# Performance work log

Hardware: AMD Instinct MI355X
Metric: run time of the kernel (lower is better)

## Reference

```python
import jax, jax.numpy as jnp
import numpy as np

IMG = 224          # image_size
FMAP = (56, 56)    # feature_map_dims (AdaptiveAvgPool2d((56,56)))
K_REWEIGHT = 3     # self.n_reweight
BLUR_RADIUS = 4    # KNNGaussianBlur(4): kernel 9, sigma 4


def _cdist(a, b):
    # Euclidean pairwise distance, [Na, D] x [Nb, D] -> [Na, Nb]
    a2 = jnp.sum(a * a, axis=1, keepdims=True)            # [Na,1]
    b2 = jnp.sum(b * b, axis=1, keepdims=True).T          # [1,Nb]
    d2 = a2 + b2 - 2.0 * (a @ b.T)
    return jnp.sqrt(jnp.maximum(d2, 0.0))


def _gaussian_blur(x):
    # x: [1,1,H,W]; torchvision GaussianBlur(kernel=9, sigma=4), reflect pad
    r, sigma = BLUR_RADIUS, float(BLUR_RADIUS)
    t = jnp.arange(2 * r + 1, dtype=x.dtype) - r
    g = jnp.exp(-(t * t) / (2.0 * sigma * sigma))
    g = g / jnp.sum(g)
    k2d = jnp.outer(g, g)[None, None]                     # [1,1,9,9]
    xp = jnp.pad(x, ((0, 0), (0, 0), (r, r), (r, r)), mode='reflect')
    return jax.lax.conv_general_dilated(
        xp, k2d, window_strides=(1, 1), padding='VALID',
        dimension_numbers=('NCHW', 'OIHW', 'NCHW'))


def setup_inputs() -> dict:
    key = jax.random.key(0)
    k1, k2 = jax.random.split(key)
    patch = jax.random.normal(k1, (FMAP[0] * FMAP[1], 768), dtype=jnp.float32)
    patch_lib = jax.random.normal(k2, (16384, 768), dtype=jnp.float32)
    mean = jnp.zeros((), dtype=jnp.float32)
    std = jnp.ones((), dtype=jnp.float32)
    return {"patch": patch, "patch_lib": patch_lib, "mean": mean, "std": std}


def reference(patch, patch_lib, mean, std):
    # normalization (method_name != 'Point_MAE' branch)
    p = (patch - mean) / std                               # [N, D]

    dist = _cdist(p, patch_lib)                            # [N, Nlib]
    min_val = jnp.min(dist, axis=1)                        # [N]
    min_idx = jnp.argmin(dist, axis=1)                     # [N]
    s_idx = jnp.argmax(min_val)
    s_star = jnp.max(min_val)

    m_test = p[s_idx]                                      # [D]
    m_star = patch_lib[min_idx[s_idx]]                     # [D]

    # distances of m_star to whole bank, k smallest
    w_dist = jnp.sqrt(jnp.maximum(
        jnp.sum((patch_lib - m_star) ** 2, axis=1), 0.0))  # [Nlib]
    _, nn_idx = jax.lax.top_k(-w_dist, K_REWEIGHT)         # smallest k
    m_star_knn = jnp.linalg.norm(
        m_test[None, :] - patch_lib[nn_idx[1:]], axis=1)   # [k-1]

    D_sqrt = jnp.sqrt(jnp.asarray(patch.shape[1], dtype=p.dtype))
    w = 1.0 - jnp.exp(s_star / D_sqrt) / jnp.sum(jnp.exp(m_star_knn / D_sqrt))
    s = w * s_star

    s_map = min_val.reshape(1, 1, *FMAP)
    s_map = jax.image.resize(s_map, (1, 1, IMG, IMG), method='bilinear')
    s_map = _gaussian_blur(s_map)
    return s, s_map
```

## Files before the change

kernel.cpp:

```cpp
#include <hip/hip_runtime.h>
#include <hip/hip_bf16.h>
#include <stdint.h>

#define N_PATCH 3136
#define N_PATCH_PAD 3328
#define N_LIB   16384
#define DIM     768
#define IMGSZ   224
#define FM      56

#define TILE 256
#define BK 32
#define KT 24
#define MT 13
#define NTILES 64

#define TAILB 64
#define D2_MARGIN 8.0f

typedef __bf16 bf16_t;
typedef __bf16 bf16x8 __attribute__((ext_vector_type(8)));
typedef __bf16 bf16x4_v __attribute__((ext_vector_type(4)));
typedef float  f32x4  __attribute__((ext_vector_type(4)));

#define FLT_MAX_ 3.402823466e+38f

struct Scal {
  unsigned long long approx_max_pack;
  unsigned long long cand_pack[64];
  int cand[64];
  int cand_count;
  int bar[4];
};

__device__ __forceinline__ float wave_reduce_sum(float v) {
#pragma unroll
  for (int s = 32; s > 0; s >>= 1) v += __shfl_xor(v, s, 64);
  return v;
}

__device__ __forceinline__ float wave_reduce_min(float v) {
#pragma unroll
  for (int s = 32; s > 0; s >>= 1) v = fminf(v, __shfl_xor(v, s, 64));
  return v;
}

__device__ __forceinline__ unsigned long long shfl_xor_u64(unsigned long long v, int mask) {
  unsigned lo = (unsigned)v, hi = (unsigned)(v >> 32);
  lo = __shfl_xor(lo, mask, 64);
  hi = __shfl_xor(hi, mask, 64);
  return ((unsigned long long)hi << 32) | lo;
}

__device__ __forceinline__ void async16(const bf16_t* g, bf16_t* l) {
  __builtin_amdgcn_global_load_lds(
      (const __attribute__((address_space(1))) unsigned int*)g,
      (__attribute__((address_space(3))) unsigned int*)l, 16, 0, 0);
}

__device__ __forceinline__ void grid_bar(int* ctr, int nb) {
  __syncthreads();
  if (threadIdx.x == 0) {
    __threadfence();
    atomicAdd(ctr, 1);
    while (atomicAdd(ctr, 0) < nb) __builtin_amdgcn_s_sleep(8);
    __threadfence();
  }
  __syncthreads();
}

__device__ __forceinline__ float bf16u_to_f(unsigned short u) {
  return __uint_as_float(((unsigned)u) << 16);
}

__global__ void prep_kernel(const float* __restrict__ patch, const float* __restrict__ lib,
                            const float* __restrict__ meanp, const float* __restrict__ stdp,
                            bf16_t* __restrict__ pb, bf16_t* __restrict__ lb,
                            float* __restrict__ a2, float* __restrict__ b2, Scal* sc) {
  int t = threadIdx.x;
  int lane = t & 63;
  if (blockIdx.x == 0) {
    if (t < 64) sc->cand_pack[t] = ~0ULL;
    if (t == 64) { sc->approx_max_pack = 0ULL; sc->cand_count = 0; }
    if (t >= 65 && t < 69) sc->bar[t - 65] = 0;
  }
  if (blockIdx.x < N_PATCH / 4) {
    int row = blockIdx.x * 4 + (t >> 6);
    float mu = meanp[0], sd = stdp[0];
    float acc = 0.f;
#pragma unroll
    for (int k = 0; k < 3; k++) {
      float4 v = ((const float4*)(patch + (size_t)row * DIM))[lane + 64 * k];
      v.x = (v.x - mu) / sd; v.y = (v.y - mu) / sd;
      v.z = (v.z - mu) / sd; v.w = (v.w - mu) / sd;
      bf16x4_v o = {(__bf16)v.x, (__bf16)v.y, (__bf16)v.z, (__bf16)v.w};
      *(bf16x4_v*)(pb + (size_t)row * DIM + (lane + 64 * k) * 4) = o;
      acc += v.x*v.x + v.y*v.y + v.z*v.z + v.w*v.w;
    }
    acc = wave_reduce_sum(acc);
    if (lane == 0) a2[row] = acc;
  } else {
    int row = (blockIdx.x - N_PATCH / 4) * 4 + (t >> 6);
    float acc = 0.f;
#pragma unroll
    for (int k = 0; k < 3; k++) {
      float4 v = ((const float4*)(lib + (size_t)row * DIM))[lane + 64 * k];
      bf16x4_v o = {(__bf16)v.x, (__bf16)v.y, (__bf16)v.z, (__bf16)v.w};
      *(bf16x4_v*)(lb + (size_t)row * DIM + (lane + 64 * k) * 4) = o;
      acc += v.x*v.x + v.y*v.y + v.z*v.z + v.w*v.w;
    }
    acc = wave_reduce_sum(acc);
    if (lane == 0) b2[row] = acc;
  }
}

__global__ __launch_bounds__(512, 2)
void gemm_min_kernel(const bf16_t* __restrict__ pb, const bf16_t* __restrict__ lb,
                     const float* __restrict__ a2, const float* __restrict__ b2,
                     float* __restrict__ part) {
  __shared__ __align__(16) bf16_t As[4][TILE * BK];
  __shared__ __align__(16) bf16_t Bs[4][TILE * BK];

  const int t = threadIdx.x;
  const int wave = t >> 6;
  const int lane = t & 63;
  const int l15 = lane & 15;
  const int quad = lane >> 4;
  const int wm = (wave >> 2) * 128;
  const int wn = (wave & 3) * 64;

  const int lid = blockIdx.x;
  const int xcd = lid & 7;
  const int slot = lid >> 3;
  const int ntile = xcd + 8 * (slot / MT);
  const int mtile = slot % MT;
  const int m0 = mtile * TILE;
  const int n0 = ntile * TILE;

  int ra0 = m0 + (t >> 2);        if (ra0 > N_PATCH - 1) ra0 = N_PATCH - 1;
  int ra1 = m0 + 128 + (t >> 2);  if (ra1 > N_PATCH - 1) ra1 = N_PATCH - 1;
  const bf16_t* gA0 = pb + (size_t)ra0 * DIM + (t & 3) * 8;
  const bf16_t* gA1 = pb + (size_t)ra1 * DIM + (t & 3) * 8;
  const bf16_t* gB0 = lb + (size_t)(n0 + (t >> 2)) * DIM + (t & 3) * 8;
  const bf16_t* gB1 = gB0 + (size_t)128 * DIM;

  auto stage = [&](int kt, int s) {
    const size_t ko = (size_t)kt * BK;
    async16(gA0 + ko, &As[s][0] + (size_t)t * 8);
    async16(gA1 + ko, &As[s][0] + 4096 + (size_t)t * 8);
    async16(gB0 + ko, &Bs[s][0] + (size_t)t * 8);
    async16(gB1 + ko, &Bs[s][0] + 4096 + (size_t)t * 8);
  };

  f32x4 acc[8][4];
#pragma unroll
  for (int mi = 0; mi < 8; mi++)
#pragma unroll
    for (int ni = 0; ni < 4; ni++) { f32x4 z = {0.f,0.f,0.f,0.f}; acc[mi][ni] = z; }

  stage(0, 0); stage(1, 1); stage(2, 2);

  auto compute = [&](int s) {
    const bf16_t* Ab = &As[s][0];
    const bf16_t* Bb = &Bs[s][0];
    bf16x8 afr[8], bfr[4];
#pragma unroll
    for (int ni = 0; ni < 4; ni++)
      bfr[ni] = *(const bf16x8*)(Bb + (wn + ni * 16 + l15) * BK + quad * 8);
#pragma unroll
    for (int mi = 0; mi < 8; mi++)
      afr[mi] = *(const bf16x8*)(Ab + (wm + mi * 16 + l15) * BK + quad * 8);
    __builtin_amdgcn_s_setprio(1);
#pragma unroll
    for (int mi = 0; mi < 8; mi++)
#pragma unroll
      for (int ni = 0; ni < 4; ni++)
        acc[mi][ni] = __builtin_amdgcn_mfma_f32_16x16x32_bf16(afr[mi], bfr[ni],
                                                              acc[mi][ni], 0, 0, 0);
    __builtin_amdgcn_s_setprio(0);
  };

  for (int k = 0; k < KT - 3; ++k) {
    asm volatile("s_waitcnt vmcnt(8)" ::: "memory");
    __builtin_amdgcn_s_barrier();
    asm volatile("" ::: "memory");
    stage(k + 3, (k + 3) & 3);
    compute(k & 3);
  }
  asm volatile("s_waitcnt vmcnt(8)" ::: "memory");
  __builtin_amdgcn_s_barrier();
  asm volatile("" ::: "memory");
  compute((KT - 3) & 3);

  asm volatile("s_waitcnt vmcnt(4)" ::: "memory");
  __builtin_amdgcn_s_barrier();
  asm volatile("" ::: "memory");
  compute((KT - 2) & 3);

  asm volatile("s_waitcnt vmcnt(0)" ::: "memory");
  __builtin_amdgcn_s_barrier();
  asm volatile("" ::: "memory");
  compute((KT - 1) & 3);

  __syncthreads();
  unsigned* smin = (unsigned*)&As[0][0];
  if (t < 256) smin[t] = 0xffffffffu;
  __syncthreads();

  float b2n[4];
#pragma unroll
  for (int ni = 0; ni < 4; ni++) b2n[ni] = b2[n0 + wn + ni * 16 + l15];

#pragma unroll
  for (int mi = 0; mi < 8; mi++) {
#pragma unroll
    for (int r = 0; r < 4; r++) {
      int rloc = wm + mi * 16 + quad * 4 + r;
      int mrow = m0 + rloc;
      float a2v = a2[mrow < N_PATCH ? mrow : (N_PATCH - 1)];
      float best = a2v + b2n[0] - 2.0f * acc[mi][0][r];
#pragma unroll
      for (int ni = 1; ni < 4; ni++)
        best = fminf(best, a2v + b2n[ni] - 2.0f * acc[mi][ni][r]);
      best = fmaxf(best, 0.0f);
#pragma unroll
      for (int s = 1; s < 16; s <<= 1)
        best = fminf(best, __shfl_xor(best, s, 64));
      if (l15 == 0) atomicMin(&smin[rloc], __float_as_uint(best));
    }
  }
  __syncthreads();
  if (t < 256) part[(size_t)ntile * N_PATCH_PAD + m0 + t] = __uint_as_float(smin[t]);
}

__device__ __forceinline__ void wave_pick(const Scal* sc, int cnt, int lane,
                                          int* srow, float* sstar, int* ms) {
  unsigned long long pk = 0ULL;
  int rowv = 0, msv = 0;
  if (lane < cnt) {
    unsigned long long cp = sc->cand_pack[lane];
    rowv = sc->cand[lane];
    msv = (int)(cp & 0xffffffffu);
    pk = (cp & 0xffffffff00000000ULL) | (unsigned)(0xffffffffu - (unsigned)rowv);
  }
  unsigned long long m = pk;
#pragma unroll
  for (int s = 1; s < 64; s <<= 1) {
    unsigned long long o = shfl_xor_u64(m, s);
    if (o > m) m = o;
  }
  unsigned long long mask = __ballot(pk == m && lane < cnt);
  int wl = (int)(__ffsll((long long)mask) - 1);
  *srow = __shfl(rowv, wl, 64);
  *ms   = __shfl(msv, wl, 64);
  *sstar = sqrtf(__uint_as_float((unsigned)(m >> 32)));
}

__global__ __launch_bounds__(256, 2)
void tail_kernel(const float* __restrict__ part, float* __restrict__ min_val,
                 const float* __restrict__ patch, const float* __restrict__ lib,
                 const bf16_t* __restrict__ lb,
                 const float* __restrict__ meanp, const float* __restrict__ stdp,
                 Scal* __restrict__ sc, float* __restrict__ wdist2,
                 float* __restrict__ out0, float* __restrict__ outmap) {
  __shared__ union {
    unsigned long long sl[768];
    float rs[40 * 40];
  } sm;
  __shared__ float redbuf[4];
  __shared__ int s_cnt;

  const int t = threadIdx.x;
  const int b = blockIdx.x;
  const int wave = t >> 6, lane = t & 63;

  {
    int row = b * 256 + t;
    if (row < N_PATCH) {
      float m = FLT_MAX_;
#pragma unroll 8
      for (int nt = 0; nt < NTILES; nt++)
        m = fminf(m, part[(size_t)nt * N_PATCH_PAD + row]);
      float v = sqrtf(m);
      min_val[row] = v;
      unsigned long long mp = (((unsigned long long)__float_as_uint(v)) << 32) |
                              (unsigned)(0xffffffffu - (unsigned)row);
      atomicMax(&sc->approx_max_pack, mp);
    }
  }
  grid_bar(&sc->bar[0], TAILB);

  if (b == 0) {
    float amax = __uint_as_float((unsigned)(atomicMax(&sc->approx_max_pack, 0ULL) >> 32));
    for (int i = t; i < N_PATCH; i += 256) {
      if (min_val[i] >= amax - 0.05f) {
        int p = atomicAdd(&sc->cand_count, 1);
        if (p < 64) sc->cand[p] = i;
      }
    }
  }
  grid_bar(&sc->bar[1], TAILB);

  if (t == 0) s_cnt = atomicAdd(&sc->cand_count, 0);
  __syncthreads();
  int cnt = s_cnt; if (cnt > 64) cnt = 64;

  {
    float mu = meanp[0], sd = stdp[0];
    for (int c = 0; c < cnt; c++) {
      int row = sc->cand[c];
      float pv_ = (t < NTILES) ? part[(size_t)t * N_PATCH_PAD + row] : FLT_MAX_;
      pv_ = wave_reduce_min(pv_);
      if (lane == 0) redbuf[wave] = pv_;
      __syncthreads();
      float bmin = fminf(fminf(redbuf[0], redbuf[1]), fminf(redbuf[2], redbuf[3]));
      __syncthreads();

      float4 pv[3];
#pragma unroll
      for (int k = 0; k < 3; k++) {
        float4 v = ((const float4*)(patch + (size_t)row * DIM))[lane + 64 * k];
        v.x = (v.x - mu) / sd; v.y = (v.y - mu) / sd;
        v.z = (v.z - mu) / sd; v.w = (v.w - mu) / sd;
        pv[k] = v;
      }
      int nt = b;
      float pmin = part[(size_t)nt * N_PATCH_PAD + row];
      if (pmin <= bmin + D2_MARGIN) {
        unsigned long long best = ~0ULL;
        int jb = nt * 256 + wave * 64;
        for (int rr = 0; rr < 64; rr++) {
          int j = jb + rr;
          const float4* pl = (const float4*)(lib + (size_t)j * DIM);
          float acc = 0.f;
#pragma unroll
          for (int k = 0; k < 3; k++) {
            float4 l = pl[lane + 64 * k];
            float dx = pv[k].x - l.x, dy = pv[k].y - l.y;
            float dz = pv[k].z - l.z, dw = pv[k].w - l.w;
            acc += dx*dx + dy*dy + dz*dz + dw*dw;
          }
          acc = wave_reduce_sum(acc);
          unsigned long long pk = (((unsigned long long)__float_as_uint(acc)) << 32) | (unsigned)j;
          if (pk < best) best = pk;
        }
        if (lane == 0) atomicMin(&sc->cand_pack[c], best);
      }
    }
  }
  grid_bar(&sc->bar[2], TAILB);

  {
    int srow_, ms; float ss_;
    wave_pick(sc, cnt, lane, &srow_, &ss_, &ms);
    float pm[12];
    const ushort4* pms = (const ushort4*)(lb + (size_t)ms * DIM);
#pragma unroll
    for (int k = 0; k < 3; k++) {
      ushort4 u = pms[lane + 64 * k];
      pm[k*4+0] = bf16u_to_f(u.x); pm[k*4+1] = bf16u_to_f(u.y);
      pm[k*4+2] = bf16u_to_f(u.z); pm[k*4+3] = bf16u_to_f(u.w);
    }
    int jbase = b * 256 + wave * 64;
    for (int rr = 0; rr < 64; rr += 2) {
      int j0 = jbase + rr, j1 = j0 + 1;
      const ushort4* r0 = (const ushort4*)(lb + (size_t)j0 * DIM);
      const ushort4* r1 = (const ushort4*)(lb + (size_t)j1 * DIM);
      float a0 = 0.f, a1 = 0.f;
#pragma unroll
      for (int k = 0; k < 3; k++) {
        ushort4 u0 = r0[lane + 64 * k];
        ushort4 u1 = r1[lane + 64 * k];
        float d;
        d = bf16u_to_f(u0.x) - pm[k*4+0]; a0 += d * d;
        d = bf16u_to_f(u0.y) - pm[k*4+1]; a0 += d * d;
        d = bf16u_to_f(u0.z) - pm[k*4+2]; a0 += d * d;
        d = bf16u_to_f(u0.w) - pm[k*4+3]; a0 += d * d;
        d = bf16u_to_f(u1.x) - pm[k*4+0]; a1 += d * d;
        d = bf16u_to_f(u1.y) - pm[k*4+1]; a1 += d * d;
        d = bf16u_to_f(u1.z) - pm[k*4+2]; a1 += d * d;
        d = bf16u_to_f(u1.w) - pm[k*4+3]; a1 += d * d;
      }
      a0 = wave_reduce_sum(a0);
      a1 = wave_reduce_sum(a1);
      if (lane == 0) { wdist2[j0] = a0; wdist2[j1] = a1; }
    }
  }
  grid_bar(&sc->bar[3], TAILB);

  if (b == 0) {
    unsigned long long b0 = ~0ULL, b1 = ~0ULL, b2 = ~0ULL;
    for (int j = t; j < N_LIB; j += 256) {
      unsigned long long pk = (((unsigned long long)__float_as_uint(wdist2[j])) << 32) | (unsigned)j;
      if (pk < b0)      { b2 = b1; b1 = b0; b0 = pk; }
      else if (pk < b1) { b2 = b1; b1 = pk; }
      else if (pk < b2) { b2 = pk; }
    }
    sm.sl[t * 3 + 0] = b0; sm.sl[t * 3 + 1] = b1; sm.sl[t * 3 + 2] = b2;
    __syncthreads();
    if (t >= 64) return;

    unsigned long long c0 = ~0ULL, c1 = ~0ULL, c2 = ~0ULL;
#pragma unroll
    for (int e = 0; e < 12; e++) {
      unsigned long long pk = sm.sl[t * 12 + e];
      if (pk < c0)      { c2 = c1; c1 = c0; c0 = pk; }
      else if (pk < c1) { c2 = c1; c1 = pk; }
      else if (pk < c2) { c2 = pk; }
    }
    unsigned long long res1 = 0, res2 = 0;
#pragma unroll
    for (int r = 0; r < 3; r++) {
      unsigned long long m = c0;
#pragma unroll
      for (int s = 1; s < 64; s <<= 1) {
        unsigned long long o = shfl_xor_u64(m, s);
        if (o < m) m = o;
      }
      if (r == 1) res1 = m;
      if (r == 2) res2 = m;
      if (c0 == m) { c0 = c1; c1 = c2; c2 = ~0ULL; }
    }
    int nA = (int)(res1 & 0xffffffffu);
    int nB = (int)(res2 & 0xffffffffu);

    int srow, ms2; float sstar;
    wave_pick(sc, cnt, t, &srow, &sstar, &ms2);

    float mu = meanp[0], sd = stdp[0];
    float accA = 0.f, accB = 0.f;
#pragma unroll
    for (int k = 0; k < 3; k++) {
      float4 p4 = ((const float4*)(patch + (size_t)srow * DIM))[t + 64 * k];
      float4 a4 = ((const float4*)(lib + (size_t)nA * DIM))[t + 64 * k];
      float4 b4 = ((const float4*)(lib + (size_t)nB * DIM))[t + 64 * k];
      float px = (p4.x - mu) / sd, py = (p4.y - mu) / sd;
      float pz = (p4.z - mu) / sd, pw = (p4.w - mu) / sd;
      float dax = px - a4.x, day = py - a4.y, daz = pz - a4.z, daw = pw - a4.w;
      float dbx = px - b4.x, dby = py - b4.y, dbz = pz - b4.z, dbw = pw - b4.w;
      accA += dax*dax + day*day + daz*daz + daw*daw;
      accB += dbx*dbx + dby*dby + dbz*dbz + dbw*dbw;
    }
    accA = wave_reduce_sum(accA);
    accB = wave_reduce_sum(accB);
    if (t == 0) {
      float dsq = sqrtf((float)DIM);
      float d1 = sqrtf(accA), d2v = sqrtf(accB);
      float w = 1.0f - expf(sstar / dsq) / (expf(d1 / dsq) + expf(d2v / dsq));
      out0[0] = w * sstar;
    }
    return;
  }

  if (b > 49) return;
  {
    int tile = b - 1;
    int bx = tile % 7, by = tile / 7;
    int ox0 = bx * 32, oy0 = by * 32;

    for (int i = t; i < 1600; i += 256) {
      int ly = i / 40, lx = i % 40;
      int gy = oy0 - 4 + ly; gy = gy < 0 ? 0 : (gy > 223 ? 223 : gy);
      int gx = ox0 - 4 + lx; gx = gx < 0 ? 0 : (gx > 223 ? 223 : gx);
      float sy = fminf(fmaxf(0.25f * gy - 0.375f, 0.0f), 55.0f);
      float sx = fminf(fmaxf(0.25f * gx - 0.375f, 0.0f), 55.0f);
      int y0 = (int)sy; if (y0 > 54) y0 = 54;
      int x0 = (int)sx; if (x0 > 54) x0 = 54;
      float fy = sy - y0, fx = sx - x0;
      float v00 = min_val[y0*FM + x0],     v01 = min_val[y0*FM + x0 + 1];
      float v10 = min_val[(y0+1)*FM + x0], v11 = min_val[(y0+1)*FM + x0 + 1];
      float a = v00 + fx * (v01 - v00);
      float bb = v10 + fx * (v11 - v10);
      sm.rs[i] = a + fy * (bb - a);
    }
    __syncthreads();

    float g[9]; float gs = 0.f;
#pragma unroll
    for (int i = 0; i < 9; i++) { float tt = (float)(i - 4); g[i] = expf(-(tt*tt)/32.0f); gs += g[i]; }
#pragma unroll
    for (int i = 0; i < 9; i++) g[i] /= gs;

    for (int p = t; p < 1024; p += 256) {
      int y = oy0 + p / 32, x = ox0 + (p & 31);
      float acc = 0.f;
#pragma unroll
      for (int dy = 0; dy < 9; dy++) {
        int yy = y + dy - 4;
        yy = yy < 0 ? -yy : (yy > IMGSZ - 1 ? 2*(IMGSZ-1) - yy : yy);
        int lyy = yy - (oy0 - 4);
        float ra = 0.f;
#pragma unroll
        for (int dx = 0; dx < 9; dx++) {
          int xx = x + dx - 4;
          xx = xx < 0 ? -xx : (xx > IMGSZ - 1 ? 2*(IMGSZ-1) - xx : xx);
          ra += g[dx] * sm.rs[lyy * 40 + (xx - (ox0 - 4))];
        }
        acc += g[dy] * ra;
      }
      outmap[y * IMGSZ + x] = acc;
    }
  }
}

extern "C" void kernel_launch(void* const* d_in, const int* in_sizes, int n_in,
                              void* d_out, int out_size, void* d_ws, size_t ws_size,
                              hipStream_t stream) {
  const float* patch = (const float*)d_in[0];
  const float* lib   = (const float*)d_in[1];
  const float* meanp = (const float*)d_in[2];
  const float* stdp  = (const float*)d_in[3];
  float* out = (float*)d_out;

  char* ws = (char*)d_ws;
  size_t off = 0;
  auto alloc = [&](size_t bytes) -> void* {
    void* p = ws + off;
    off = (off + bytes + 255) & ~(size_t)255;
    return p;
  };
  bf16_t* pb      = (bf16_t*)alloc((size_t)N_PATCH * DIM * sizeof(bf16_t));
  bf16_t* lb      = (bf16_t*)alloc((size_t)N_LIB * DIM * sizeof(bf16_t));
  float* a2       = (float*)alloc(N_PATCH * sizeof(float));
  float* b2       = (float*)alloc(N_LIB * sizeof(float));
  float* part     = (float*)alloc((size_t)N_PATCH_PAD * NTILES * sizeof(float));
  float* min_val  = (float*)alloc(N_PATCH * sizeof(float));
  float* wdist2   = (float*)alloc(N_LIB * sizeof(float));
  Scal*  sc       = (Scal*)alloc(sizeof(Scal));

  prep_kernel<<<N_PATCH / 4 + N_LIB / 4, 256, 0, stream>>>(patch, lib, meanp, stdp,
                                                           pb, lb, a2, b2, sc);
  gemm_min_kernel<<<MT * NTILES, 512, 0, stream>>>(pb, lb, a2, b2, part);
  tail_kernel<<<TAILB, 256, 0, stream>>>(part, min_val, patch, lib, lb, meanp, stdp,
                                         sc, wdist2, out, out + 1);
}
```

Measured before the change: 349.5 us.

## Make GEMM-min kernel persistent with BK=64 swizzled LDS and interleaved quadrant pipeline

Turns the distance GEMM into a persistent kernel with 256 blocks, each looping over output tiles in an XCD-aware order. The K-step grows to 64 and uses double-buffered LDS with an XOR-swizzled layout to avoid bank conflicts. Each step is split into four quadrant MFMA phases, with per-half async loads interleaved between barriers. The goal is to cut launch and tail overhead, LDS bank conflicts and load stalls, at the cost of more barriers and only two pipeline stages.

```diff
diff --git a/kernel.cpp b/kernel.cpp
--- a/kernel.cpp
+++ b/kernel.cpp
@@ -10,8 +10,7 @@
 #define FM      56
 
 #define TILE 256
-#define BK 32
-#define KT 24
+#define KT2 12
 #define MT 13
 #define NTILES 64
 
@@ -24,6 +23,10 @@
 typedef float  f32x4  __attribute__((ext_vector_type(4)));
 
 #define FLT_MAX_ 3.402823466e+38f
+
+#define BARF() do { asm volatile("" ::: "memory"); \
+                    __builtin_amdgcn_s_barrier();  \
+                    asm volatile("" ::: "memory"); } while (0)
 
 struct Scal {
   unsigned long long approx_max_pack;
@@ -31,6 +34,7 @@
   int cand[64];
   int cand_count;
   int bar[4];
+  int work;
 };
 
 __device__ __forceinline__ float wave_reduce_sum(float v) {
@@ -83,6 +87,7 @@
     if (t < 64) sc->cand_pack[t] = ~0ULL;
     if (t == 64) { sc->approx_max_pack = 0ULL; sc->cand_count = 0; }
     if (t >= 65 && t < 69) sc->bar[t - 65] = 0;
+    if (t == 69) sc->work = 0;
   }
   if (blockIdx.x < N_PATCH / 4) {
     int row = blockIdx.x * 4 + (t >> 6);
@@ -118,8 +123,8 @@
 void gemm_min_kernel(const bf16_t* __restrict__ pb, const bf16_t* __restrict__ lb,
                      const float* __restrict__ a2, const float* __restrict__ b2,
                      float* __restrict__ part) {
-  __shared__ __align__(16) bf16_t As[4][TILE * BK];
-  __shared__ __align__(16) bf16_t Bs[4][TILE * BK];
+  __shared__ __align__(16) bf16_t As[2][2][128 * 64];
+  __shared__ __align__(16) bf16_t Bs[2][2][128 * 64];
 
   const int t = threadIdx.x;
   const int wave = t >> 6;
@@ -128,109 +133,161 @@
   const int quad = lane >> 4;
   const int wm = (wave >> 2) * 128;
   const int wn = (wave & 3) * 64;
-
-  const int lid = blockIdx.x;
-  const int xcd = lid & 7;
-  const int slot = lid >> 3;
-  const int ntile = xcd + 8 * (slot / MT);
-  const int mtile = slot % MT;
-  const int m0 = mtile * TILE;
-  const int n0 = ntile * TILE;
-
-  int ra0 = m0 + (t >> 2);        if (ra0 > N_PATCH - 1) ra0 = N_PATCH - 1;
-  int ra1 = m0 + 128 + (t >> 2);  if (ra1 > N_PATCH - 1) ra1 = N_PATCH - 1;
-  const bf16_t* gA0 = pb + (size_t)ra0 * DIM + (t & 3) * 8;
-  const bf16_t* gA1 = pb + (size_t)ra1 * DIM + (t & 3) * 8;
-  const bf16_t* gB0 = lb + (size_t)(n0 + (t >> 2)) * DIM + (t & 3) * 8;
-  const bf16_t* gB1 = gB0 + (size_t)128 * DIM;
-
-  auto stage = [&](int kt, int s) {
-    const size_t ko = (size_t)kt * BK;
-    async16(gA0 + ko, &As[s][0] + (size_t)t * 8);
-    async16(gA1 + ko, &As[s][0] + 4096 + (size_t)t * 8);
-    async16(gB0 + ko, &Bs[s][0] + (size_t)t * 8);
-    async16(gB1 + ko, &Bs[s][0] + 4096 + (size_t)t * 8);
-  };
-
-  f32x4 acc[8][4];
-#pragma unroll
-  for (int mi = 0; mi < 8; mi++)
-#pragma unroll
-    for (int ni = 0; ni < 4; ni++) { f32x4 z = {0.f,0.f,0.f,0.f}; acc[mi][ni] = z; }
-
-  stage(0, 0); stage(1, 1); stage(2, 2);
-
-  auto compute = [&](int s) {
-    const bf16_t* Ab = &As[s][0];
-    const bf16_t* Bb = &Bs[s][0];
-    bf16x8 afr[8], bfr[4];
-#pragma unroll
-    for (int ni = 0; ni < 4; ni++)
-      bfr[ni] = *(const bf16x8*)(Bb + (wn + ni * 16 + l15) * BK + quad * 8);
+  const int mhw = wm >> 7;
+  const int nhw = wn >> 7;
+  const int wni = wn & 64;
+
+  const int L0 = t >> 3,      k0 = (t & 7) ^ (L0 & 7);
+  const int L1 = 64 + (t >> 3), k1 = (t & 7) ^ (L1 & 7);
+  const int sl0 = (((0 * 4 + quad) ^ (l15 & 7)) << 4);
+  const int sl1 = (((1 * 4 + quad) ^ (l15 & 7)) << 4);
+
+  const int x = blockIdx.x & 7;
+  const int sblk = blockIdx.x >> 3;
+
+  for (int ii = sblk; ii < 104; ii += 32) {
+    const int nt = x * 8 + ii / 13;
+    const int mt = ii % 13;
+    const int m0 = mt * TILE;
+    const int n0 = nt * TILE;
+
+    __syncthreads();
+
+    int rA00 = m0 + L0;        if (rA00 > N_PATCH - 1) rA00 = N_PATCH - 1;
+    int rA01 = m0 + L1;        if (rA01 > N_PATCH - 1) rA01 = N_PATCH - 1;
+    int rA10 = m0 + 128 + L0;  if (rA10 > N_PATCH - 1) rA10 = N_PATCH - 1;
+    int rA11 = m0 + 128 + L1;  if (rA11 > N_PATCH - 1) rA11 = N_PATCH - 1;
+    const bf16_t* gA00 = pb + (size_t)rA00 * DIM + k0 * 8;
+    const bf16_t* gA01 = pb + (size_t)rA01 * DIM + k1 * 8;
+    const bf16_t* gA10 = pb + (size_t)rA10 * DIM + k0 * 8;
+    const bf16_t* gA11 = pb + (size_t)rA11 * DIM + k1 * 8;
+    const bf16_t* gB00 = lb + (size_t)(n0 + L0) * DIM + k0 * 8;
+    const bf16_t* gB01 = lb + (size_t)(n0 + L1) * DIM + k1 * 8;
+    const bf16_t* gB10 = lb + (size_t)(n0 + 128 + L0) * DIM + k0 * 8;
+    const bf16_t* gB11 = lb + (size_t)(n0 + 128 + L1) * DIM + k1 * 8;
+
+    auto stageA = [&](int tk, int mh) {
+      bf16_t* dst = &As[tk & 1][mh][0];
+      const bf16_t* s0 = mh ? gA10 : gA00;
+      const bf16_t* s1 = mh ? gA11 : gA01;
+      async16(s0 + tk * 64, dst + t * 8);
+      async16(s1 + tk * 64, dst + 4096 + t * 8);
+    };
+    auto stageB = [&](int tk, int nh) {
+      bf16_t* dst = &Bs[tk & 1][nh][0];
+      const bf16_t* s0 = nh ? gB10 : gB00;
+      const bf16_t* s1 = nh ? gB11 : gB01;
+      async16(s0 + tk * 64, dst + t * 8);
+      async16(s1 + tk * 64, dst + 4096 + t * 8);
+    };
+
+    f32x4 acc[8][4];
 #pragma unroll
     for (int mi = 0; mi < 8; mi++)
-      afr[mi] = *(const bf16x8*)(Ab + (wm + mi * 16 + l15) * BK + quad * 8);
-    __builtin_amdgcn_s_setprio(1);
-#pragma unroll
-    for (int mi = 0; mi < 8; mi++)
-#pragma unroll
-      for (int ni = 0; ni < 4; ni++)
-        acc[mi][ni] = __builtin_amdgcn_mfma_f32_16x16x32_bf16(afr[mi], bfr[ni],
-                                                              acc[mi][ni], 0, 0, 0);
-    __builtin_amdgcn_s_setprio(0);
-  };
-
-  for (int k = 0; k < KT - 3; ++k) {
-    asm volatile("s_waitcnt vmcnt(8)" ::: "memory");
-    __builtin_amdgcn_s_barrier();
-    asm volatile("" ::: "memory");
-    stage(k + 3, (k + 3) & 3);
-    compute(k & 3);
-  }
-  asm volatile("s_waitcnt vmcnt(8)" ::: "memory");
-  __builtin_amdgcn_s_barrier();
-  asm volatile("" ::: "memory");
-  compute((KT - 3) & 3);
-
-  asm volatile("s_waitcnt vmcnt(4)" ::: "memory");
-  __builtin_amdgcn_s_barrier();
-  asm volatile("" ::: "memory");
-  compute((KT - 2) & 3);
-
-  asm volatile("s_waitcnt vmcnt(0)" ::: "memory");
-  __builtin_amdgcn_s_barrier();
-  asm volatile("" ::: "memory");
-  compute((KT - 1) & 3);
-
-  __syncthreads();
-  unsigned* smin = (unsigned*)&As[0][0];
-  if (t < 256) smin[t] = 0xffffffffu;
-  __syncthreads();
-
-  float b2n[4];
-#pragma unroll
-  for (int ni = 0; ni < 4; ni++) b2n[ni] = b2[n0 + wn + ni * 16 + l15];
-
-#pragma unroll
-  for (int mi = 0; mi < 8; mi++) {
-#pragma unroll
-    for (int r = 0; r < 4; r++) {
-      int rloc = wm + mi * 16 + quad * 4 + r;
-      int mrow = m0 + rloc;
-      float a2v = a2[mrow < N_PATCH ? mrow : (N_PATCH - 1)];
-      float best = a2v + b2n[0] - 2.0f * acc[mi][0][r];
-#pragma unroll
-      for (int ni = 1; ni < 4; ni++)
-        best = fminf(best, a2v + b2n[ni] - 2.0f * acc[mi][ni][r]);
-      best = fmaxf(best, 0.0f);
-#pragma unroll
-      for (int s = 1; s < 16; s <<= 1)
-        best = fminf(best, __shfl_xor(best, s, 64));
-      if (l15 == 0) atomicMin(&smin[rloc], __float_as_uint(best));
-    }
-  }
-  __syncthreads();
-  if (t < 256) part[(size_t)ntile * N_PATCH_PAD + m0 + t] = __uint_as_float(smin[t]);
+#pragma unroll
+      for (int ni = 0; ni < 4; ni++) { f32x4 z = {0.f,0.f,0.f,0.f}; acc[mi][ni] = z; }
+
+    bf16x8 afr[4][2], b0f[2][2], b1f[2][2];
+
+    auto readA = [&](int d, int mh) {
+      const char* base = (const char*)&As[d][mhw][0];
+#pragma unroll
+      for (int mi = 0; mi < 4; mi++) {
+        int lr = mh * 64 + mi * 16 + l15;
+        afr[mi][0] = *(const bf16x8*)(base + lr * 128 + sl0);
+        afr[mi][1] = *(const bf16x8*)(base + lr * 128 + sl1);
+      }
+    };
+    auto readB = [&](int d, int nh, bf16x8 (&bf)[2][2]) {
+      const char* base = (const char*)&Bs[d][nhw][0];
+#pragma unroll
+      for (int ni = 0; ni < 2; ni++) {
+        int lr = wni + nh * 32 + ni * 16 + l15;
+        bf[ni][0] = *(const bf16x8*)(base + lr * 128 + sl0);
+        bf[ni][1] = *(const bf16x8*)(base + lr * 128 + sl1);
+      }
+    };
+    auto mfq = [&](int mh, int nh, bf16x8 (&bf)[2][2]) {
+      __builtin_amdgcn_s_setprio(1);
+#pragma unroll
+      for (int mi = 0; mi < 4; mi++)
+#pragma unroll
+        for (int ni = 0; ni < 2; ni++) {
+          acc[mh*4+mi][nh*2+ni] = __builtin_amdgcn_mfma_f32_16x16x32_bf16(
+              afr[mi][0], bf[ni][0], acc[mh*4+mi][nh*2+ni], 0, 0, 0);
+          acc[mh*4+mi][nh*2+ni] = __builtin_amdgcn_mfma_f32_16x16x32_bf16(
+              afr[mi][1], bf[ni][1], acc[mh*4+mi][nh*2+ni], 0, 0, 0);
+        }
+      __builtin_amdgcn_s_setprio(0);
+    };
+
+    auto half_iter = [&](int d, int tst, bool stg) {
+      if (stg) {
+        stageA(tst, 0);
+        asm volatile("s_waitcnt vmcnt(2)" ::: "memory");
+      } else {
+        asm volatile("s_waitcnt vmcnt(0)" ::: "memory");
+      }
+      BARF();
+      readB(d, 0, b0f);
+      readA(d, 0);
+      mfq(0, 0, b0f);
+      BARF();
+      readB(d, 1, b1f);
+      if (stg) stageA(tst, 1);
+      BARF();
+      mfq(0, 1, b1f);
+      BARF();
+      readA(d, 1);
+      if (stg) stageB(tst, 0);
+      BARF();
+      mfq(1, 1, b1f);
+      BARF();
+      if (stg) stageB(tst, 1);
+      BARF();
+      mfq(1, 0, b0f);
+      BARF();
+    };
+
+    stageA(0, 0); stageA(0, 1); stageB(0, 0); stageB(0, 1);
+
+    for (int tt = 0; tt < 10; tt += 2) {
+      half_iter(0, tt + 1, true);
+      half_iter(1, tt + 2, true);
+    }
+    half_iter(0, 11, true);
+    half_iter(1, 12, false);
+
+    __syncthreads();
+    unsigned* smin = (unsigned*)&As[0][0][0];
+    if (t < 256) smin[t] = 0xffffffffu;
+    __syncthreads();
+
+    float b2n[4];
+#pragma unroll
+    for (int ni = 0; ni < 4; ni++) b2n[ni] = b2[n0 + wn + ni * 16 + l15];
+
+#pragma unroll
+    for (int mi = 0; mi < 8; mi++) {
+#pragma unroll
+      for (int r = 0; r < 4; r++) {
+        int rloc = wm + mi * 16 + quad * 4 + r;
+        int mrow = m0 + rloc;
+        float a2v = a2[mrow < N_PATCH ? mrow : (N_PATCH - 1)];
+        float best = a2v + b2n[0] - 2.0f * acc[mi][0][r];
+#pragma unroll
+        for (int ni = 1; ni < 4; ni++)
+          best = fminf(best, a2v + b2n[ni] - 2.0f * acc[mi][ni][r]);
+        best = fmaxf(best, 0.0f);
+#pragma unroll
+        for (int s = 1; s < 16; s <<= 1)
+          best = fminf(best, __shfl_xor(best, s, 64));
+        if (l15 == 0) atomicMin(&smin[rloc], __float_as_uint(best));
+      }
+    }
+    __syncthreads();
+    if (t < 256) part[(size_t)nt * N_PATCH_PAD + m0 + t] = __uint_as_float(smin[t]);
+  }
 }
 
 __device__ __forceinline__ void wave_pick(const Scal* sc, int cnt, int lane,
@@ -530,7 +587,7 @@
 
   prep_kernel<<<N_PATCH / 4 + N_LIB / 4, 256, 0, stream>>>(patch, lib, meanp, stdp,
                                                            pb, lb, a2, b2, sc);
-  gemm_min_kernel<<<MT * NTILES, 512, 0, stream>>>(pb, lb, a2, b2, part);
+  gemm_min_kernel<<<256, 512, 0, stream>>>(pb, lb, a2, b2, part);
   tail_kernel<<<TAILB, 256, 0, stream>>>(part, min_val, patch, lib, lb, meanp, stdp,
                                          sc, wdist2, out, out + 1);
 }
```

After: 333.5 us. 1.05x faster.
